# Performance work log

Measured on AMD Instinct MI355X. Metric: run time of the kernel, lower is better.

## Reference

```python
import jax, jax.numpy as jnp
import numpy as np

N, D, A, NQ, G1, G2 = 2048, 512, 64, 8, 8, 8
A1 = 2 * A  # tier-1 MQA uses att_dim*2 internally


def setup_inputs() -> dict:
    key = jax.random.key(0)
    ks = iter(jax.random.split(key, 24))
    r = lambda *sh: (jax.random.normal(next(ks), sh, dtype=jnp.float32) * 0.02)
    return {
        "x": jax.random.normal(next(ks), (N, D), dtype=jnp.float32),
        # tier 1 (num_groups_first MQA blocks, inner dim A1)
        "Wq1": r(G1, NQ, D, A1), "bq1": r(G1, NQ, A1),
        "Wk1": r(G1, D, A1),     "bk1": r(G1, A1),
        "Wv1": r(G1, D, A1),     "bv1": r(G1, A1),
        "Wo1": r(G1, NQ * A1, D), "bo1": r(G1, D),
        # tier 2 (num_groups_second MQA blocks, inner dim A)
        "Wq2": r(G2, NQ, D, A), "bq2": r(G2, NQ, A),
        "Wk2": r(G2, D, A),     "bk2": r(G2, A),
        "Wv2": r(G2, D, A),     "bv2": r(G2, A),
        "Wo2": r(G2, NQ * A, D), "bo2": r(G2, D),
        # final projection: in = att_dim * num_groups_second == D
        "Wo": r(D, D), "bo": r(D),
    }


def _mqa_grouped(xg, Wq, bq, Wk, bk, Wv, bv, Wo, bo):
    """Batched MultiQueryAttention over a group axis g.
    xg: [g, n, d]; Wq: [g, q, d, a]. No softmax (per source)."""
    a = Wq.shape[-1]
    q = jnp.einsum('gnd,gqda->gqna', xg, Wq) + bq[:, :, None, :]
    k = jnp.einsum('gnd,gda->gna', xg, Wk) + bk[:, None, :]
    v = jnp.einsum('gnd,gda->gna', xg, Wv) + bv[:, None, :]
    scores = jnp.einsum('gqna,gma->gqnm', q, k) / jnp.sqrt(jnp.asarray(a, jnp.float32))
    ctx = jnp.einsum('gqnm,gma->gqna', scores, v)          # [g,q,n,a]
    g, nq, n, ad = ctx.shape
    ctx = ctx.transpose(0, 2, 1, 3).reshape(g, n, nq * ad)  # concat queries on feat dim
    return jnp.einsum('gnf,gfd->gnd', ctx, Wo) + bo[:, None, :]


def reference(x, Wq1, bq1, Wk1, bk1, Wv1, bv1, Wo1, bo1,
              Wq2, bq2, Wk2, bk2, Wv2, bv2, Wo2, bo2, Wo, bo):
    xg = jnp.broadcast_to(x[None], (G1, N, D))
    o1 = _mqa_grouped(xg, Wq1, bq1, Wk1, bk1, Wv1, bv1, Wo1, bo1)   # [G1,N,D]
    o2 = _mqa_grouped(o1[:G2], Wq2, bq2, Wk2, bk2, Wv2, bv2, Wo2, bo2)  # [G2,N,D]
    o2_flat = o2.reshape(G2 * N, D)  # torch.cat along token dim (dim=0)
    return o2_flat @ Wo + bo          # [G2*N, D]
```

## Files before the change

### kernel.cpp

```cpp
#include <hip/hip_runtime.h>


typedef __bf16 bf16x8 __attribute__((ext_vector_type(8)));
typedef float  f32x4  __attribute__((ext_vector_type(4)));

struct PD { const float* s; void* d; int R, C, Bc, mode, blocks; };
struct PArgs { PD p[20]; int n; };

struct MA {
    const float *x,*bq1,*bo1,*bq2,*bo2,*bo;
    float* out;
    __bf16 *xb,*Wk1t,*Wv1t,*Wq1b,*Wo1t,*Wk2t,*Wv2t,*Wq2b,*Wo2b,*Wot;
    __bf16 *Ktb,*Vtb,*T1b,*M1t,*o1b,*K2tb,*V2tb,*T2b,*Wo2pT,*M2pt;
    float *STf1,*STf2,*kvb1,*kvb2,*c1,*c2p,*bo2p;
    PArgs pa;
    int prepTot;
};

template<int BM, int BN, int KK>
__device__ __forceinline__ void ss_gemm(void* smv,
    const __bf16* __restrict__ A, const float* __restrict__ Bf,
    __bf16* __restrict__ C, long aG, long bG, long cG, int cD, int cQ, int vb)
{
    constexpr int MT = BM / 32, NT = BN / 32, KS = KK / 32;
    constexpr int ACH = (KK * 2) / 16;
    constexpr int ABYTES = BM * KK * 2;
    constexpr int AITER = ABYTES / 16 / 256;
    constexpr int ROWB = KK * 2;
    constexpr int F4PT = (BN * KK) / 4 / 256;
    constexpr int TPR  = (KK / 4) / F4PT;

    char* smc = (char*)smv;
    int g = vb >> 6, rb = vb & 63;
    A  += g * aG + (long)rb * BM * KK;
    Bf += g * bG;
    C  += g * cG;

    int tid = threadIdx.x, wave = tid >> 6, lane = tid & 63;
    int mrow = lane & 15, quad = lane >> 4;

    #pragma unroll
    for (int i = 0; i < AITER; ++i) {
        int c = tid + i * 256;
        int row = c / ACH, cp = c % ACH;
        int cg = cp ^ (row & 7);
        __builtin_amdgcn_global_load_lds(
            (const __attribute__((address_space(1))) void*)(A + (long)row * KK + cg * 8),
            (__attribute__((address_space(3))) void*)(smc + c * 16),
            16, 0, 0);
    }
    {
        int brow = tid / TPR, bseg = tid % TPR;
        const float4* bsrc = (const float4*)(Bf + (long)brow * KK + bseg * (KK / TPR));
        int cbase = (bseg * (KK / TPR)) >> 3;
        int bx7 = brow & 7;
        char* bls = smc + ABYTES + (long)brow * ROWB;
        #pragma unroll
        for (int j = 0; j < F4PT / 2; ++j) {
            float4 f0 = bsrc[2 * j], f1 = bsrc[2 * j + 1];
            bf16x8 v = {(__bf16)f0.x, (__bf16)f0.y, (__bf16)f0.z, (__bf16)f0.w,
                        (__bf16)f1.x, (__bf16)f1.y, (__bf16)f1.z, (__bf16)f1.w};
            *(bf16x8*)(bls + (((cbase + j) ^ bx7) << 4)) = v;
        }
    }
    __syncthreads();

    int wm = (wave >> 1) * (BM / 2), wn = (wave & 1) * (BN / 2);
    f32x4 acc[MT][NT];
    #pragma unroll
    for (int i = 0; i < MT; ++i)
        #pragma unroll
        for (int j = 0; j < NT; ++j)
            acc[i][j] = f32x4{0.f, 0.f, 0.f, 0.f};

    #pragma unroll
    for (int ks = 0; ks < KS; ++ks) {
        bf16x8 af[MT], bv[NT];
        #pragma unroll
        for (int mt = 0; mt < MT; ++mt) {
            int r = wm + mt * 16 + mrow;
            af[mt] = *(const bf16x8*)(smc + (long)r * ROWB
                        + (((ks * 4 + quad) ^ (r & 7)) << 4));
        }
        #pragma unroll
        for (int nt = 0; nt < NT; ++nt) {
            int r = wn + nt * 16 + mrow;
            bv[nt] = *(const bf16x8*)(smc + ABYTES + (long)r * ROWB
                        + (((ks * 4 + quad) ^ (r & 7)) << 4));
        }
        #pragma unroll
        for (int mt = 0; mt < MT; ++mt)
            #pragma unroll
            for (int nt = 0; nt < NT; ++nt)
                acc[mt][nt] = __builtin_amdgcn_mfma_f32_16x16x32_bf16(
                    af[mt], bv[nt], acc[mt][nt], 0, 0, 0);
    }

    #pragma unroll
    for (int mt = 0; mt < MT; ++mt) {
        #pragma unroll
        for (int r4 = 0; r4 < 4; ++r4) {
            int rl = wm + mt * 16 + quad * 4 + r4;
            int ra = rb * BM + rl;
            int q = ra >> 9, d = ra & 511;
            #pragma unroll
            for (int nt = 0; nt < NT; ++nt) {
                int col = wn + nt * 16 + mrow;
                C[(long)d * cD + q * cQ + col] = (__bf16)acc[mt][nt][r4];
            }
        }
    }
}

template<int BM, int BN, bool BF32>
__device__ __forceinline__ void gemm_block(void* smv,
    const __bf16* __restrict__ A, const void* __restrict__ Bv,
    const float* __restrict__ bias, void* __restrict__ Cv,
    int K, int lda, int ldb, int ldc, int divq, int ksplit,
    long aOut, long aIn, long bOut, long bIn, long cOut, long cIn,
    long biasOut, long biasIn, int hasBias, int mode, float alpha,
    int bx, int by, int bz)
{
    constexpr int MT = BM / 32, NT = BN / 32;
    constexpr int HALF = (BM + BN) * 64;
    constexpr int AL = BM / 64;
    constexpr int BL = BF32 ? 0 : BN / 64;

    char* smc = (char*)smv;

    int b  = bz / ksplit, ks = bz - b * ksplit;
    int go = b / divq,  gi = b - go * divq;
    A += go * aOut + gi * aIn;
    const __bf16* Bb = (const __bf16*)Bv + (BF32 ? 0 : (go * bOut + gi * bIn));
    const float*  Bf = (const float*)Bv + (BF32 ? (go * bOut + gi * bIn) : 0);
    long cBase = go * cOut + gi * cIn;
    if (hasBias) bias += go * biasOut + gi * biasIn;

    int kChunk = K / ksplit;
    int k0 = ks * kChunk;
    int nT = kChunk / 32;

    int bm = by * BM, bn = bx * BN;
    int tid = threadIdx.x, wave = tid >> 6, lane = tid & 63;
    int wm = (wave >> 1) * (BM / 2), wn = (wave & 1) * (BN / 2);
    int mrow = lane & 15, quad = lane >> 4;

    f32x4 acc[MT][NT];
    #pragma unroll
    for (int i = 0; i < MT; ++i)
        #pragma unroll
        for (int j = 0; j < NT; ++j)
            acc[i][j] = f32x4{0.f, 0.f, 0.f, 0.f};

    float4 bf0, bf1;
    int brow = tid >> 2, bcb = (tid & 3) * 8;

    auto loadBf32 = [&](int kk) {
        const float* src = Bf + (long)(bn + brow) * ldb + kk + bcb;
        bf0 = *(const float4*)(src);
        bf1 = *(const float4*)(src + 4);
    };
    auto writeBf32 = [&](int buf) {
        bf16x8 v = {(__bf16)bf0.x, (__bf16)bf0.y, (__bf16)bf0.z, (__bf16)bf0.w,
                    (__bf16)bf1.x, (__bf16)bf1.y, (__bf16)bf1.z, (__bf16)bf1.w};
        *(bf16x8*)(smc + buf * HALF + BM * 64 + brow * 64 + bcb * 2) = v;
    };
    auto issueAB = [&](int buf, int kk) {
        char* base = smc + buf * HALF;
        #pragma unroll
        for (int t = 0; t < AL; ++t) {
            int c = tid + t * 256;
            int row = c >> 2, kq = c & 3;
            __builtin_amdgcn_global_load_lds(
                (const __attribute__((address_space(1))) void*)
                    (A + (long)(bm + row) * lda + kk + kq * 8),
                (__attribute__((address_space(3))) void*)(base + row * 64 + kq * 16),
                16, 0, 0);
        }
        if constexpr (!BF32) {
            #pragma unroll
            for (int t = 0; t < BL; ++t) {
                int c = tid + t * 256;
                int row = c >> 2, kq = c & 3;
                __builtin_amdgcn_global_load_lds(
                    (const __attribute__((address_space(1))) void*)
                        (Bb + (long)(bn + row) * ldb + kk + kq * 8),
                    (__attribute__((address_space(3))) void*)
                        (base + BM * 64 + row * 64 + kq * 16),
                    16, 0, 0);
            }
        }
    };

    if constexpr (BF32) loadBf32(k0);
    issueAB(0, k0);
    if constexpr (BF32) writeBf32(0);
    __syncthreads();

    int cur = 0;
    for (int t = 0; t < nT; ++t) {
        int kk = k0 + (t + 1) * 32;
        if (t + 1 < nT) {
            if constexpr (BF32) loadBf32(kk);
            issueAB(cur ^ 1, kk);
        }

        char* base = smc + cur * HALF;
        bf16x8 af[MT], bfv[NT];
        #pragma unroll
        for (int mt = 0; mt < MT; ++mt)
            af[mt] = *(const bf16x8*)(base + (wm + mt * 16 + mrow) * 64 + quad * 16);
        #pragma unroll
        for (int nt = 0; nt < NT; ++nt)
            bfv[nt] = *(const bf16x8*)(base + BM * 64 + (wn + nt * 16 + mrow) * 64 + quad * 16);
        #pragma unroll
        for (int mt = 0; mt < MT; ++mt)
            #pragma unroll
            for (int nt = 0; nt < NT; ++nt)
                acc[mt][nt] = __builtin_amdgcn_mfma_f32_16x16x32_bf16(
                    af[mt], bfv[nt], acc[mt][nt], 0, 0, 0);

        if constexpr (BF32) {
            if (t + 1 < nT) writeBf32(cur ^ 1);
        }

        __syncthreads();
        cur ^= 1;
    }

    #pragma unroll
    for (int mt = 0; mt < MT; ++mt) {
        #pragma unroll
        for (int r = 0; r < 4; ++r) {
            int row = bm + wm + mt * 16 + quad * 4 + r;
            #pragma unroll
            for (int nt = 0; nt < NT; ++nt) {
                int col = bn + wn + nt * 16 + mrow;
                float v = acc[mt][nt][r] * alpha;
                if (hasBias) v += bias[col];
                if (mode == 0)
                    ((float*)Cv)[cBase + (long)row * ldc + col] = v;
                else if (mode == 1)
                    ((__bf16*)Cv)[cBase + (long)row * ldc + col] = (__bf16)v;
                else if (mode == 2)
                    ((__bf16*)Cv)[cBase + (long)col * ldc + row] = (__bf16)v;
                else
                    atomicAdd(&((float*)Cv)[cBase + (long)row * ldc + col], v);
            }
        }
    }
}

__device__ __forceinline__ void prep_block(const PArgs& a, int bid, void* smv)
{
    int i = 0;
    while (i < a.n && bid >= a.p[i].blocks) { bid -= a.p[i].blocks; ++i; }
    if (i >= a.n) return;
    PD d = a.p[i];
    int t = threadIdx.x;
    if (d.mode == 0) {
        float (*tile)[33] = (float(*)[33])smv;
        int tC = d.C >> 5, tR = d.R >> 5;
        int batch = bid / (tC * tR), rem = bid - batch * (tC * tR);
        int tyo = rem / tC, txo = rem - tyo * tC;
        const float* src = d.s + (long)batch * d.R * d.C;
        __bf16* dst = (__bf16*)d.d + (long)batch * d.R * d.C;
        int tx = t & 31, ty = t >> 5;
        int r0 = tyo * 32, c0 = txo * 32;
        #pragma unroll
        for (int u = 0; u < 4; ++u)
            tile[ty + 8 * u][tx] = src[(long)(r0 + ty + 8 * u) * d.C + c0 + tx];
        __syncthreads();
        #pragma unroll
        for (int u = 0; u < 4; ++u)
            dst[(long)(c0 + ty + 8 * u) * d.R + r0 + tx] = (__bf16)tile[tx][ty + 8 * u];
    } else if (d.mode == 1) {
        long idx = ((long)bid * 256 + t) * 4;
        long total = (long)d.Bc * d.R * d.C;
        if (idx < total) {
            float4 f = *(const float4*)(d.s + idx);
            __bf16* o = (__bf16*)d.d + idx;
            o[0] = (__bf16)f.x; o[1] = (__bf16)f.y;
            o[2] = (__bf16)f.z; o[3] = (__bf16)f.w;
        }
    } else {
        long idx = (long)bid * 256 + t;
        long total = (long)d.Bc * d.R * d.C;
        if (idx < total) {
            float* o = (float*)d.d;
            if (d.mode == 2) o[idx] = d.s[idx];
            else             o[idx] = 0.f;
        }
    }
}

__device__ __forceinline__ void small_block(void* smv,
    const float* __restrict__ STf, const float* __restrict__ bq,
    const __bf16* __restrict__ WoT, const float* __restrict__ boA,
    float* __restrict__ cOut, int ad, int F, long wG, int bid)
{
    int tid = threadIdx.x;
    float* rL  = (float*)smv;
    float* red = (float*)((char*)smv + 4096);
    int g = bid >> 5, slice = bid & 31;
    int nq = F / ad;
    const float* Sg = STf + (long)g * ad * ad;
    for (int f = tid; f < F; f += 256) {
        int q = f / ad, aa = f - q * ad;
        const float* bv = bq + (long)(g * nq + q) * ad;
        const float* Sa = Sg + (long)aa * ad;
        float s = 0.f;
        for (int c = 0; c < ad; c += 4) {
            float4 b4 = *(const float4*)(bv + c);
            float4 s4 = *(const float4*)(Sa + c);
            s += b4.x * s4.x + b4.y * s4.y + b4.z * s4.z + b4.w * s4.w;
        }
        rL[f] = s;
    }
    __syncthreads();
    int dl = tid & 15, fs = tid >> 4;
    int d = slice * 16 + dl;
    int fchunk = F >> 4;
    const __bf16* wrow = WoT + (long)g * wG + (long)d * F;
    float s = 0.f;
    for (int f0 = fs * fchunk; f0 < (fs + 1) * fchunk; f0 += 8) {
        bf16x8 w = *(const bf16x8*)(wrow + f0);
        s += rL[f0]     * (float)w[0] + rL[f0 + 1] * (float)w[1]
           + rL[f0 + 2] * (float)w[2] + rL[f0 + 3] * (float)w[3]
           + rL[f0 + 4] * (float)w[4] + rL[f0 + 5] * (float)w[5]
           + rL[f0 + 6] * (float)w[6] + rL[f0 + 7] * (float)w[7];
    }
    red[tid] = s;
    __syncthreads();
    if (fs == 0) {
        float tsum = s;
        #pragma unroll
        for (int u = 1; u < 16; ++u) tsum += red[u * 16 + dl];
        cOut[(long)g * 512 + d] = boA[(long)g * 512 + d] + tsum;
    }
}

__device__ __forceinline__ void vecmat_block(void* smv,
    const float* __restrict__ v, const __bf16* __restrict__ WT,
    const float* __restrict__ bias, float* __restrict__ outp, int g, int slice)
{
    float* red2 = (float*)smv;
    int tid = threadIdx.x;
    int dl = tid & 15, fs = tid >> 4;
    int d = slice * 16 + dl;
    const float* vg = v + (long)g * 512;
    const __bf16* wrow = WT + (long)d * 512;
    float s = 0.f;
    for (int f0 = fs * 32; f0 < (fs + 1) * 32; f0 += 8) {
        bf16x8 w = *(const bf16x8*)(wrow + f0);
        s += vg[f0]     * (float)w[0] + vg[f0 + 1] * (float)w[1]
           + vg[f0 + 2] * (float)w[2] + vg[f0 + 3] * (float)w[3]
           + vg[f0 + 4] * (float)w[4] + vg[f0 + 5] * (float)w[5]
           + vg[f0 + 6] * (float)w[6] + vg[f0 + 7] * (float)w[7];
    }
    red2[tid] = s;
    __syncthreads();
    if (fs == 0) {
        float tsum = s;
        #pragma unroll
        for (int u = 1; u < 16; ++u) tsum += red2[u * 16 + dl];
        outp[(long)g * 512 + d] = bias[d] + tsum;
    }
}

template<int S>
__device__ __forceinline__ void run_stage(const MA& a, int vb, void* sm)
{
    const float isa1 = 0.08838834764831845f;
    if constexpr (S == 0) {
        prep_block(a.pa, vb, sm);
    } else if constexpr (S == 1) {
        if (vb < 1024)
            gemm_block<64,64,false>(sm, a.xb, a.Wk1t, a.kvb1, a.Ktb,
                512, 512, 512, 2048, 1, 1,
                0L, 0L, 65536L, 0L, 262144L, 0L, 128L, 0L, 1, 2, 1.0f,
                vb & 1, (vb >> 1) & 31, vb >> 6);
        else if (vb < 1536) {
            int v = vb - 1024;
            gemm_block<64,64,false>(sm, a.Wo2b, a.Wot, nullptr, a.Wo2pT,
                512, 512, 512, 512, 1, 1,
                262144L, 0L, 0L, 0L, 262144L, 0L, 0L, 0L, 0, 2, 1.0f,
                v & 7, (v >> 3) & 7, v >> 6);
        } else {
            int v = vb - 1536;
            vecmat_block(sm, a.bo2, a.Wot, a.bo, a.bo2p, v & 7, v >> 3);
        }
    } else if constexpr (S == 2) {
        gemm_block<64,64,false>(sm, a.Vtb, a.Ktb, nullptr, a.STf1,
            2048, 2048, 2048, 128, 1, 8,
            262144L, 0L, 262144L, 0L, 16384L, 0L, 0L, 0L, 0, 3, isa1,
            vb & 1, (vb >> 1) & 1, vb >> 2);
    } else if constexpr (S == 4) {
        gemm_block<64,64,false>(sm, a.T1b, a.Wo1t, nullptr, a.M1t,
            1024, 1024, 1024, 512, 1, 1,
            524288L, 0L, 524288L, 0L, 262144L, 0L, 0L, 0L, 0, 2, 1.0f,
            vb & 7, (vb >> 3) & 7, vb >> 6);
    } else if constexpr (S == 5) {
        gemm_block<128,128,false>(sm, a.xb, a.M1t, a.c1, a.o1b,
            512, 512, 512, 512, 1, 1,
            0L, 0L, 262144L, 0L, 1048576L, 0L, 512L, 0L, 1, 1, 1.0f,
            vb & 3, (vb >> 2) & 15, vb >> 6);
    } else if constexpr (S == 6) {
        gemm_block<64,64,false>(sm, a.o1b, a.Wk2t, a.kvb2, a.K2tb,
            512, 512, 512, 2048, 8, 1,
            0L, 1048576L, 262144L, 32768L, 1048576L, 131072L, 512L, 64L,
            1, 2, 1.0f, 0, vb & 31, vb >> 5);
    } else if constexpr (S == 7) {
        gemm_block<64,64,false>(sm, a.V2tb, a.K2tb, nullptr, a.STf2,
            2048, 2048, 2048, 64, 1, 16,
            131072L, 0L, 131072L, 0L, 4096L, 0L, 0L, 0L, 0, 3, 0.125f,
            0, 0, vb);
    } else if constexpr (S == 9) {
        gemm_block<64,64,false>(sm, a.T2b, a.Wo2pT, nullptr, a.M2pt,
            512, 512, 512, 512, 1, 1,
            262144L, 0L, 262144L, 0L, 262144L, 0L, 0L, 0L, 0, 2, 1.0f,
            vb & 7, (vb >> 3) & 7, vb >> 6);
    } else {
        gemm_block<128,128,false>(sm, a.o1b, a.M2pt, a.c2p, a.out,
            512, 512, 512, 512, 1, 1,
            1048576L, 0L, 262144L, 0L, 1048576L, 0L, 512L, 0L, 1, 0, 1.0f,
            vb & 3, (vb >> 2) & 15, vb >> 6);
    }
}

#define STAGE_KERNEL(NAME, S, SMEM)                                          \
__global__ __launch_bounds__(256, 4) void NAME(MA a)                         \
{                                                                            \
    __shared__ __align__(16) unsigned char smem[SMEM];                       \
    run_stage<S>(a, blockIdx.x, smem);                                       \
}

STAGE_KERNEL(ksg0_prep,    0, 16384)
STAGE_KERNEL(ksg1_kv1wo2p, 1, 16384)
STAGE_KERNEL(ksg2_s1t,     2, 16384)
STAGE_KERNEL(ksg4_m1t,     4, 16384)
STAGE_KERNEL(ksg5_o1,      5, 32768)
STAGE_KERNEL(ksg6_kv2,     6, 16384)
STAGE_KERNEL(ksg7_s2t,     7, 16384)
STAGE_KERNEL(ksg9_m2pt,    9, 16384)
STAGE_KERNEL(ksg10_out,   10, 32768)

__global__ __launch_bounds__(256, 4) void ksg3a_t1(MA a)
{
    __shared__ __align__(16) unsigned char smem[49152];
    ss_gemm<64,128,128>(smem, a.Wq1b, a.STf1, a.T1b,
                        524288L, 16384L, 524288L, 1024, 128, blockIdx.x);
}
__global__ __launch_bounds__(256, 4) void ksg3b_c1(MA a)
{
    __shared__ __align__(16) unsigned char smem[8192];
    small_block(smem, a.STf1, a.bq1, a.Wo1t, a.bo1, a.c1,
                128, 1024, 524288L, blockIdx.x);
}
__global__ __launch_bounds__(256, 4) void ksg8a_t2(MA a)
{
    __shared__ __align__(16) unsigned char smem[16384];
    ss_gemm<64,64,64>(smem, a.Wq2b, a.STf2, a.T2b,
                      262144L, 4096L, 262144L, 512, 64, blockIdx.x);
}
__global__ __launch_bounds__(256, 4) void ksg8b_c2p(MA a)
{
    __shared__ __align__(16) unsigned char smem[8192];
    small_block(smem, a.STf2, a.bq2, a.Wo2pT, a.bo2p, a.c2p,
                64, 512, 262144L, blockIdx.x);
}

extern "C" void kernel_launch(void* const* d_in, const int* in_sizes, int n_in,
                              void* d_out, int out_size, void* d_ws, size_t ws_size,
                              hipStream_t stream)
{
    MA ma;
    ma.x   = (const float*)d_in[0];
    const float* Wq1 = (const float*)d_in[1];  ma.bq1 = (const float*)d_in[2];
    const float* Wk1 = (const float*)d_in[3];  const float* bk1 = (const float*)d_in[4];
    const float* Wv1 = (const float*)d_in[5];  const float* bv1 = (const float*)d_in[6];
    const float* Wo1 = (const float*)d_in[7];  ma.bo1 = (const float*)d_in[8];
    const float* Wq2 = (const float*)d_in[9];  ma.bq2 = (const float*)d_in[10];
    const float* Wk2 = (const float*)d_in[11]; const float* bk2 = (const float*)d_in[12];
    const float* Wv2 = (const float*)d_in[13]; const float* bv2 = (const float*)d_in[14];
    const float* Wo2 = (const float*)d_in[15]; ma.bo2 = (const float*)d_in[16];
    const float* Wo  = (const float*)d_in[17]; ma.bo  = (const float*)d_in[18];
    ma.out = (float*)d_out;
    (void)in_sizes; (void)n_in; (void)out_size; (void)ws_size;

    __bf16* wb = (__bf16*)d_ws;
    long o = 0;
    ma.xb    = wb + o; o += 1048576;
    ma.Wk1t  = wb + o; o += 524288;
    ma.Wv1t  = wb + o; o += 524288;
    ma.Wq1b  = wb + o; o += 4194304;
    ma.Wo1t  = wb + o; o += 4194304;
    ma.Wk2t  = wb + o; o += 262144;
    ma.Wv2t  = wb + o; o += 262144;
    ma.Wq2b  = wb + o; o += 2097152;
    ma.Wo2b  = wb + o; o += 2097152;
    ma.Wot   = wb + o; o += 262144;
    ma.Ktb   = wb + o; o += 2097152;
    ma.Vtb   = wb + o; o += 2097152;
    ma.T1b   = wb + o; o += 4194304;
    ma.M1t   = wb + o; o += 2097152;
    ma.o1b   = wb + o; o += 8388608;
    ma.K2tb  = ma.Ktb;
    ma.V2tb  = ma.Ktb + 1048576;
    ma.T2b   = wb + o; o += 2097152;
    ma.Wo2pT = wb + o; o += 2097152;
    ma.M2pt  = wb + o; o += 2097152;
    float* wf = (float*)(wb + o);
    long p = 0;
    ma.STf1 = wf + p; p += 131072;
    ma.STf2 = wf + p; p += 32768;
    ma.kvb1 = wf + p; p += 2048;
    ma.kvb2 = wf + p; p += 1024;
    ma.c1   = wf + p; p += 4096;
    ma.c2p  = wf + p; p += 4096;
    ma.bo2p = wf + p; p += 4096;

    int nd = 0, totB = 0;
    auto add = [&](const float* s, void* d, int R, int C, int Bc, int mode) {
        int blocks;
        long total = (long)Bc * R * C;
        if (mode == 0) blocks = Bc * (R >> 5) * (C >> 5);
        else if (mode == 1) blocks = (int)(total / 1024);
        else blocks = (int)((total + 255) / 256);
        ma.pa.p[nd] = PD{s, d, R, C, Bc, mode, blocks};
        ++nd; totB += blocks;
    };
    add(ma.x, ma.xb,   2048, 512, 1, 1);
    add(Wq1,  ma.Wq1b, 512, 128, 64, 1);
    add(Wq2,  ma.Wq2b, 512, 64, 64, 1);
    add(Wo2,  ma.Wo2b, 512, 512, 8, 1);
    add(Wk1,  ma.Wk1t, 512, 128, 8, 0);
    add(Wv1,  ma.Wv1t, 512, 128, 8, 0);
    add(Wo1,  ma.Wo1t, 1024, 512, 8, 0);
    add(Wk2,  ma.Wk2t, 512, 64, 8, 0);
    add(Wv2,  ma.Wv2t, 512, 64, 8, 0);
    add(Wo,   ma.Wot,  512, 512, 1, 0);
    add(bk1,  ma.kvb1,        1, 1024, 1, 2);
    add(bv1,  ma.kvb1 + 1024, 1, 1024, 1, 2);
    add(bk2,  ma.kvb2,        1, 512, 1, 2);
    add(bv2,  ma.kvb2 + 512,  1, 512, 1, 2);
    add(nullptr, ma.STf1, 1, 131072, 1, 4);
    add(nullptr, ma.STf2, 1, 32768, 1, 4);
    ma.pa.n = nd;
    ma.prepTot = totB;

    ksg0_prep   <<<dim3(ma.prepTot), dim3(256), 0, stream>>>(ma);
    ksg1_kv1wo2p<<<dim3(1792), dim3(256), 0, stream>>>(ma);
    ksg2_s1t    <<<dim3(256),  dim3(256), 0, stream>>>(ma);
    ksg3a_t1    <<<dim3(512),  dim3(256), 0, stream>>>(ma);
    ksg3b_c1    <<<dim3(256),  dim3(256), 0, stream>>>(ma);
    ksg4_m1t    <<<dim3(512),  dim3(256), 0, stream>>>(ma);
    ksg5_o1     <<<dim3(512),  dim3(256), 0, stream>>>(ma);
    ksg6_kv2    <<<dim3(512),  dim3(256), 0, stream>>>(ma);
    ksg7_s2t    <<<dim3(128),  dim3(256), 0, stream>>>(ma);
    ksg8a_t2    <<<dim3(512),  dim3(256), 0, stream>>>(ma);
    ksg8b_c2p   <<<dim3(256),  dim3(256), 0, stream>>>(ma);
    ksg9_m2pt   <<<dim3(512),  dim3(256), 0, stream>>>(ma);
    ksg10_out   <<<dim3(512),  dim3(256), 0, stream>>>(ma);
}
```

Measured before the change: 277.7 us.

## Merge independent stage kernels and make GEMM epilogue mode compile-time with coalesced transposed stores

Two pairs of independent kernels (T1/c1 and T2/c2p) are each merged into a single launch, with blocks split by index, which cuts launch count and lets their work overlap. The GEMM output mode becomes a template parameter, so the epilogue branches are resolved at compile time. For the transposed-store mode, the MFMA operands are swapped so that adjacent lanes write adjacent addresses in the transposed output, which should give coalesced bf16 stores. The merged kernels use the larger shared memory size of the pair, which may lower occupancy for the smaller small_block half.

```diff
diff --git a/kernel.cpp b/kernel.cpp
--- a/kernel.cpp
+++ b/kernel.cpp
@@ -112,13 +112,13 @@
     }
 }
 
-template<int BM, int BN, bool BF32>
+template<int BM, int BN, bool BF32, int MODE>
 __device__ __forceinline__ void gemm_block(void* smv,
     const __bf16* __restrict__ A, const void* __restrict__ Bv,
     const float* __restrict__ bias, void* __restrict__ Cv,
     int K, int lda, int ldb, int ldc, int divq, int ksplit,
     long aOut, long aIn, long bOut, long bIn, long cOut, long cIn,
-    long biasOut, long biasIn, int hasBias, int mode, float alpha,
+    long biasOut, long biasIn, int hasBias, float alpha,
     int bx, int by, int bz)
 {
     constexpr int MT = BM / 32, NT = BN / 32;
@@ -216,9 +216,14 @@
         #pragma unroll
         for (int mt = 0; mt < MT; ++mt)
             #pragma unroll
-            for (int nt = 0; nt < NT; ++nt)
-                acc[mt][nt] = __builtin_amdgcn_mfma_f32_16x16x32_bf16(
-                    af[mt], bfv[nt], acc[mt][nt], 0, 0, 0);
+            for (int nt = 0; nt < NT; ++nt) {
+                if constexpr (MODE == 2)
+                    acc[mt][nt] = __builtin_amdgcn_mfma_f32_16x16x32_bf16(
+                        bfv[nt], af[mt], acc[mt][nt], 0, 0, 0);
+                else
+                    acc[mt][nt] = __builtin_amdgcn_mfma_f32_16x16x32_bf16(
+                        af[mt], bfv[nt], acc[mt][nt], 0, 0, 0);
+            }
 
         if constexpr (BF32) {
             if (t + 1 < nT) writeBf32(cur ^ 1);
@@ -228,24 +233,39 @@
         cur ^= 1;
     }
 
-    #pragma unroll
-    for (int mt = 0; mt < MT; ++mt) {
-        #pragma unroll
-        for (int r = 0; r < 4; ++r) {
-            int row = bm + wm + mt * 16 + quad * 4 + r;
+    if constexpr (MODE == 2) {
+        #pragma unroll
+        for (int nt = 0; nt < NT; ++nt) {
             #pragma unroll
-            for (int nt = 0; nt < NT; ++nt) {
-                int col = bn + wn + nt * 16 + mrow;
-                float v = acc[mt][nt][r] * alpha;
-                if (hasBias) v += bias[col];
-                if (mode == 0)
-                    ((float*)Cv)[cBase + (long)row * ldc + col] = v;
-                else if (mode == 1)
-                    ((__bf16*)Cv)[cBase + (long)row * ldc + col] = (__bf16)v;
-                else if (mode == 2)
-                    ((__bf16*)Cv)[cBase + (long)col * ldc + row] = (__bf16)v;
-                else
-                    atomicAdd(&((float*)Cv)[cBase + (long)row * ldc + col], v);
+            for (int r = 0; r < 4; ++r) {
+                int ci = bn + wn + nt * 16 + quad * 4 + r;
+                #pragma unroll
+                for (int mt = 0; mt < MT; ++mt) {
+                    int mi = bm + wm + mt * 16 + mrow;
+                    float v = acc[mt][nt][r] * alpha;
+                    if (hasBias) v += bias[ci];
+                    ((__bf16*)Cv)[cBase + (long)ci * ldc + mi] = (__bf16)v;
+                }
+            }
+        }
+    } else {
+        #pragma unroll
+        for (int mt = 0; mt < MT; ++mt) {
+            #pragma unroll
+            for (int r = 0; r < 4; ++r) {
+                int row = bm + wm + mt * 16 + quad * 4 + r;
+                #pragma unroll
+                for (int nt = 0; nt < NT; ++nt) {
+                    int col = bn + wn + nt * 16 + mrow;
+                    float v = acc[mt][nt][r] * alpha;
+                    if (hasBias) v += bias[col];
+                    if constexpr (MODE == 0)
+                        ((float*)Cv)[cBase + (long)row * ldc + col] = v;
+                    else if constexpr (MODE == 1)
+                        ((__bf16*)Cv)[cBase + (long)row * ldc + col] = (__bf16)v;
+                    else
+                        atomicAdd(&((float*)Cv)[cBase + (long)row * ldc + col], v);
+                }
             }
         }
     }
@@ -376,54 +396,68 @@
         prep_block(a.pa, vb, sm);
     } else if constexpr (S == 1) {
         if (vb < 1024)
-            gemm_block<64,64,false>(sm, a.xb, a.Wk1t, a.kvb1, a.Ktb,
+            gemm_block<64,64,false,2>(sm, a.xb, a.Wk1t, a.kvb1, a.Ktb,
                 512, 512, 512, 2048, 1, 1,
-                0L, 0L, 65536L, 0L, 262144L, 0L, 128L, 0L, 1, 2, 1.0f,
+                0L, 0L, 65536L, 0L, 262144L, 0L, 128L, 0L, 1, 1.0f,
                 vb & 1, (vb >> 1) & 31, vb >> 6);
         else if (vb < 1536) {
             int v = vb - 1024;
-            gemm_block<64,64,false>(sm, a.Wo2b, a.Wot, nullptr, a.Wo2pT,
+            gemm_block<64,64,false,2>(sm, a.Wo2b, a.Wot, nullptr, a.Wo2pT,
                 512, 512, 512, 512, 1, 1,
-                262144L, 0L, 0L, 0L, 262144L, 0L, 0L, 0L, 0, 2, 1.0f,
+                262144L, 0L, 0L, 0L, 262144L, 0L, 0L, 0L, 0, 1.0f,
                 v & 7, (v >> 3) & 7, v >> 6);
         } else {
             int v = vb - 1536;
             vecmat_block(sm, a.bo2, a.Wot, a.bo, a.bo2p, v & 7, v >> 3);
         }
     } else if constexpr (S == 2) {
-        gemm_block<64,64,false>(sm, a.Vtb, a.Ktb, nullptr, a.STf1,
+        gemm_block<64,64,false,3>(sm, a.Vtb, a.Ktb, nullptr, a.STf1,
             2048, 2048, 2048, 128, 1, 8,
-            262144L, 0L, 262144L, 0L, 16384L, 0L, 0L, 0L, 0, 3, isa1,
+            262144L, 0L, 262144L, 0L, 16384L, 0L, 0L, 0L, 0, isa1,
             vb & 1, (vb >> 1) & 1, vb >> 2);
+    } else if constexpr (S == 3) {
+        if (vb < 512)
+            ss_gemm<64,128,128>(sm, a.Wq1b, a.STf1, a.T1b,
+                                524288L, 16384L, 524288L, 1024, 128, vb);
+        else
+            small_block(sm, a.STf1, a.bq1, a.Wo1t, a.bo1, a.c1,
+                        128, 1024, 524288L, vb - 512);
     } else if constexpr (S == 4) {
-        gemm_block<64,64,false>(sm, a.T1b, a.Wo1t, nullptr, a.M1t,
+        gemm_block<64,64,false,2>(sm, a.T1b, a.Wo1t, nullptr, a.M1t,
             1024, 1024, 1024, 512, 1, 1,
-            524288L, 0L, 524288L, 0L, 262144L, 0L, 0L, 0L, 0, 2, 1.0f,
+            524288L, 0L, 524288L, 0L, 262144L, 0L, 0L, 0L, 0, 1.0f,
             vb & 7, (vb >> 3) & 7, vb >> 6);
     } else if constexpr (S == 5) {
-        gemm_block<128,128,false>(sm, a.xb, a.M1t, a.c1, a.o1b,
+        gemm_block<128,128,false,1>(sm, a.xb, a.M1t, a.c1, a.o1b,
             512, 512, 512, 512, 1, 1,
-            0L, 0L, 262144L, 0L, 1048576L, 0L, 512L, 0L, 1, 1, 1.0f,
+            0L, 0L, 262144L, 0L, 1048576L, 0L, 512L, 0L, 1, 1.0f,
             vb & 3, (vb >> 2) & 15, vb >> 6);
     } else if constexpr (S == 6) {
-        gemm_block<64,64,false>(sm, a.o1b, a.Wk2t, a.kvb2, a.K2tb,
+        gemm_block<64,64,false,2>(sm, a.o1b, a.Wk2t, a.kvb2, a.K2tb,
             512, 512, 512, 2048, 8, 1,
             0L, 1048576L, 262144L, 32768L, 1048576L, 131072L, 512L, 64L,
-            1, 2, 1.0f, 0, vb & 31, vb >> 5);
+            1, 1.0f, 0, vb & 31, vb >> 5);
     } else if constexpr (S == 7) {
-        gemm_block<64,64,false>(sm, a.V2tb, a.K2tb, nullptr, a.STf2,
+        gemm_block<64,64,false,3>(sm, a.V2tb, a.K2tb, nullptr, a.STf2,
             2048, 2048, 2048, 64, 1, 16,
-            131072L, 0L, 131072L, 0L, 4096L, 0L, 0L, 0L, 0, 3, 0.125f,
+            131072L, 0L, 131072L, 0L, 4096L, 0L, 0L, 0L, 0, 0.125f,
             0, 0, vb);
+    } else if constexpr (S == 8) {
+        if (vb < 512)
+            ss_gemm<64,64,64>(sm, a.Wq2b, a.STf2, a.T2b,
+                              262144L, 4096L, 262144L, 512, 64, vb);
+        else
+            small_block(sm, a.STf2, a.bq2, a.Wo2pT, a.bo2p, a.c2p,
+                        64, 512, 262144L, vb - 512);
     } else if constexpr (S == 9) {
-        gemm_block<64,64,false>(sm, a.T2b, a.Wo2pT, nullptr, a.M2pt,
+        gemm_block<64,64,false,2>(sm, a.T2b, a.Wo2pT, nullptr, a.M2pt,
             512, 512, 512, 512, 1, 1,
-            262144L, 0L, 262144L, 0L, 262144L, 0L, 0L, 0L, 0, 2, 1.0f,
+            262144L, 0L, 262144L, 0L, 262144L, 0L, 0L, 0L, 0, 1.0f,
             vb & 7, (vb >> 3) & 7, vb >> 6);
     } else {
-        gemm_block<128,128,false>(sm, a.o1b, a.M2pt, a.c2p, a.out,
+        gemm_block<128,128,false,0>(sm, a.o1b, a.M2pt, a.c2p, a.out,
             512, 512, 512, 512, 1, 1,
-            1048576L, 0L, 262144L, 0L, 1048576L, 0L, 512L, 0L, 1, 0, 1.0f,
+            1048576L, 0L, 262144L, 0L, 1048576L, 0L, 512L, 0L, 1, 1.0f,
             vb & 3, (vb >> 2) & 15, vb >> 6);
     }
 }
@@ -438,37 +472,14 @@
 STAGE_KERNEL(ksg0_prep,    0, 16384)
 STAGE_KERNEL(ksg1_kv1wo2p, 1, 16384)
 STAGE_KERNEL(ksg2_s1t,     2, 16384)
+STAGE_KERNEL(ksg3_t1c1,    3, 49152)
 STAGE_KERNEL(ksg4_m1t,     4, 16384)
 STAGE_KERNEL(ksg5_o1,      5, 32768)
 STAGE_KERNEL(ksg6_kv2,     6, 16384)
 STAGE_KERNEL(ksg7_s2t,     7, 16384)
+STAGE_KERNEL(ksg8_t2c2p,   8, 16384)
 STAGE_KERNEL(ksg9_m2pt,    9, 16384)
 STAGE_KERNEL(ksg10_out,   10, 32768)
-
-__global__ __launch_bounds__(256, 4) void ksg3a_t1(MA a)
-{
-    __shared__ __align__(16) unsigned char smem[49152];
-    ss_gemm<64,128,128>(smem, a.Wq1b, a.STf1, a.T1b,
-                        524288L, 16384L, 524288L, 1024, 128, blockIdx.x);
-}
-__global__ __launch_bounds__(256, 4) void ksg3b_c1(MA a)
-{
-    __shared__ __align__(16) unsigned char smem[8192];
-    small_block(smem, a.STf1, a.bq1, a.Wo1t, a.bo1, a.c1,
-                128, 1024, 524288L, blockIdx.x);
-}
-__global__ __launch_bounds__(256, 4) void ksg8a_t2(MA a)
-{
-    __shared__ __align__(16) unsigned char smem[16384];
-    ss_gemm<64,64,64>(smem, a.Wq2b, a.STf2, a.T2b,
-                      262144L, 4096L, 262144L, 512, 64, blockIdx.x);
-}
-__global__ __launch_bounds__(256, 4) void ksg8b_c2p(MA a)
-{
-    __shared__ __align__(16) unsigned char smem[8192];
-    small_block(smem, a.STf2, a.bq2, a.Wo2pT, a.bo2p, a.c2p,
-                64, 512, 262144L, blockIdx.x);
-}
 
 extern "C" void kernel_launch(void* const* d_in, const int* in_sizes, int n_in,
                               void* d_out, int out_size, void* d_ws, size_t ws_size,
@@ -552,14 +563,12 @@
     ksg0_prep   <<<dim3(ma.prepTot), dim3(256), 0, stream>>>(ma);
     ksg1_kv1wo2p<<<dim3(1792), dim3(256), 0, stream>>>(ma);
     ksg2_s1t    <<<dim3(256),  dim3(256), 0, stream>>>(ma);
-    ksg3a_t1    <<<dim3(512),  dim3(256), 0, stream>>>(ma);
-    ksg3b_c1    <<<dim3(256),  dim3(256), 0, stream>>>(ma);
+    ksg3_t1c1   <<<dim3(768),  dim3(256), 0, stream>>>(ma);
     ksg4_m1t    <<<dim3(512),  dim3(256), 0, stream>>>(ma);
     ksg5_o1     <<<dim3(512),  dim3(256), 0, stream>>>(ma);
     ksg6_kv2    <<<dim3(512),  dim3(256), 0, stream>>>(ma);
     ksg7_s2t    <<<dim3(128),  dim3(256), 0, stream>>>(ma);
-    ksg8a_t2    <<<dim3(512),  dim3(256), 0, stream>>>(ma);
-    ksg8b_c2p   <<<dim3(256),  dim3(256), 0, stream>>>(ma);
+    ksg8_t2c2p  <<<dim3(768),  dim3(256), 0, stream>>>(ma);
     ksg9_m2pt   <<<dim3(512),  dim3(256), 0, stream>>>(ma);
     ksg10_out   <<<dim3(512),  dim3(256), 0, stream>>>(ma);
 }
```

Measured after the change: 267.8 us. 1.04x faster.
